# Kernel optimization log

Hardware: AMD Instinct MI355X
Metric: run time of the kernel (lower is better)

The kernel has to match this reference:

```python
import jax, jax.numpy as jnp
import numpy as np

N_NODES = 50000
N_EDGES = 800000
DIM = 128
NUM_GRAPHS = 512


def setup_inputs() -> dict:
    key = jax.random.key(0)
    ks = jax.random.split(key, 12)
    s = 1.0 / np.sqrt(DIM)
    inp = {
        'x': jax.random.normal(ks[0], (N_NODES, DIM), dtype=jnp.float32),
        'edge_index': jax.random.randint(ks[1], (2, N_EDGES), 0, N_NODES, dtype=jnp.int32),
        'batch': jnp.sort(jax.random.randint(ks[2], (N_NODES,), 0, NUM_GRAPHS, dtype=jnp.int32)),
        'W1a': jax.random.uniform(ks[3], (DIM, DIM), jnp.float32, -s, s),
        'b1a': jax.random.uniform(ks[4], (DIM,), jnp.float32, -s, s),
        'W1b': jax.random.uniform(ks[5], (DIM, DIM), jnp.float32, -s, s),
        'b1b': jax.random.uniform(ks[6], (DIM,), jnp.float32, -s, s),
        'W2a': jax.random.uniform(ks[7], (DIM, DIM), jnp.float32, -s, s),
        'b2a': jax.random.uniform(ks[8], (DIM,), jnp.float32, -s, s),
        'W2b': jax.random.uniform(ks[9], (DIM, DIM), jnp.float32, -s, s),
        'b2b': jax.random.uniform(ks[10], (DIM,), jnp.float32, -s, s),
    }
    return inp


def _gin_conv(x, edge_index, Wa, ba, Wb, bb):
    # GINConv with eps=0: h_i = MLP(x_i + sum_{j->i} x_j)
    src, dst = edge_index[0], edge_index[1]
    agg = jax.ops.segment_sum(x[src], dst, num_segments=x.shape[0])  # [N, F]
    h = x + agg
    h = jax.nn.relu(h @ Wa + ba)
    return h @ Wb + bb


def reference(x, edge_index, batch, W1a, b1a, W1b, b1b, W2a, b2a, W2b, b2b):
    h = _gin_conv(x, edge_index, W1a, b1a, W1b, b1b)
    h = _gin_conv(h, edge_index, W2a, b2a, W2b, b2b)
    # global mean pool over graphs
    sums = jax.ops.segment_sum(h, batch, num_segments=NUM_GRAPHS)      # [G, F]
    counts = jax.ops.segment_sum(jnp.ones((h.shape[0],), h.dtype), batch, num_segments=NUM_GRAPHS)
    return sums / jnp.maximum(counts, 1.0)[:, None]
```

## Files before the change

### kernel.cpp

```cpp
#include <hip/hip_runtime.h>

#define DIM 128
#define NBUCK 784
#define EPB 8192
#define ELDS_CAP 2048

typedef unsigned short ushortT;
typedef unsigned int uintT;
typedef __attribute__((ext_vector_type(8))) __bf16 bf16x8;
typedef __attribute__((ext_vector_type(4))) float f32x4;

__device__ inline ushortT f2bf(float f) {
    union { float f; uintT u; } v; v.f = f;
    uintT u = v.u;
    uintT r = (u + 0x7FFFu + ((u >> 16) & 1u)) >> 16;
    return (ushortT)r;
}
__device__ inline float bfu_lo(uintT u) { union { uintT u; float f; } v; v.u = u << 16; return v.f; }
__device__ inline float bfu_hi(uintT u) { union { uintT u; float f; } v; v.u = u & 0xffff0000u; return v.f; }
__device__ inline float bfs(ushortT s) { union { uintT u; float f; } v; v.u = ((uintT)s) << 16; return v.f; }

__device__ inline int off_in_row(int k) {
    return (((k >> 5) * 4 + ((k & 15) >> 2)) << 4) + (((k >> 4) & 1) << 3) + ((k & 3) << 1);
}

__device__ inline int wave_iscan(int v) {
    int lane = threadIdx.x & 63;
    #pragma unroll
    for (int d = 1; d < 64; d <<= 1) {
        int t = __shfl_up(v, d, 64);
        if (lane >= d) v += t;
    }
    return v;
}

__global__ __launch_bounds__(256)
void scan_blk_kernel(int* __restrict__ a, int n, int* __restrict__ bsum) {
    __shared__ int ws[4];
    const int tid = threadIdx.x;
    const int i = blockIdx.x * 256 + tid;
    const int lane = tid & 63, wv = tid >> 6;
    int v = (i < n) ? a[i] : 0;
    int isc = wave_iscan(v);
    if (lane == 63) ws[wv] = isc;
    __syncthreads();
    if (tid == 0) { int run = 0; for (int w = 0; w < 4; ++w) { int t = ws[w]; ws[w] = run; run += t; } }
    __syncthreads();
    int e = ws[wv] + isc - v;
    if (i < n) a[i] = e;
    if (tid == 255) bsum[blockIdx.x] = e + v;
}

__global__ __launch_bounds__(256)
void scan_add2_kernel(int* __restrict__ a, int n, const int* __restrict__ bsum) {
    __shared__ int ws[4];
    __shared__ int s_carry;
    const int tid = threadIdx.x;
    int partial = 0;
    for (int i = tid; i < (int)blockIdx.x; i += 256) partial += bsum[i];
    #pragma unroll
    for (int d = 1; d < 64; d <<= 1) partial += __shfl_xor(partial, d, 64);
    if ((tid & 63) == 0) ws[tid >> 6] = partial;
    __syncthreads();
    if (tid == 0) s_carry = ws[0] + ws[1] + ws[2] + ws[3];
    __syncthreads();
    int i = blockIdx.x * 256 + tid;
    if (i < n) a[i] += s_carry;
}

__global__ __launch_bounds__(256)
void histA_kernel(const int* __restrict__ dstIdx, int* __restrict__ histg, int ne, int nblk) {
    __shared__ int h[NBUCK];
    const int j = blockIdx.x;
    for (int i = threadIdx.x; i < NBUCK; i += 256) h[i] = 0;
    __syncthreads();
    const int base = j * EPB;
    const int end = (base + EPB < ne) ? base + EPB : ne;
    for (int i = base + threadIdx.x; i < end; i += 256)
        atomicAdd(&h[dstIdx[i] >> 6], 1);
    __syncthreads();
    for (int b = threadIdx.x; b < NBUCK; b += 256)
        histg[b * nblk + j] = h[b];
}

__global__ __launch_bounds__(256)
void fillA_kernel(const int* __restrict__ srcIdx, const int* __restrict__ dstIdx,
                  const int* __restrict__ Sg, uintT* __restrict__ pairs, int ne, int nblk) {
    __shared__ int cur[NBUCK];
    const int j = blockIdx.x;
    for (int i = threadIdx.x; i < NBUCK; i += 256) cur[i] = Sg[i * nblk + j];
    __syncthreads();
    const int base = j * EPB;
    const int end = (base + EPB < ne) ? base + EPB : ne;
    for (int i = base + threadIdx.x; i < end; i += 256) {
        const int d = dstIdx[i];
        const int b = d >> 6;
        const int pos = atomicAdd(&cur[b], 1);
        pairs[pos] = ((uintT)srcIdx[i] << 6) | (uintT)(d & 63);
    }
}

__global__ __launch_bounds__(256)
void convert_prep_kernel(const float* __restrict__ x, ushortT* __restrict__ xb, int n,
                         const float* __restrict__ W0, const float* __restrict__ W1,
                         const float* __restrict__ W2, const float* __restrict__ W3,
                         ushortT* __restrict__ Wt) {
    if (blockIdx.x < 128) {
        int w = blockIdx.x >> 5;
        const float* W = (w == 0) ? W0 : (w == 1) ? W1 : (w == 2) ? W2 : W3;
        ushortT* dst = Wt + (size_t)w * DIM * DIM;
        int i = (blockIdx.x & 31) * 256 + threadIdx.x;
        int nidx = i >> 6, p = i & 63, k = 2 * p;
        float w0 = W[k * DIM + nidx];
        float w1 = W[(k + 1) * DIM + nidx];
        uintT u = ((uintT)f2bf(w1) << 16) | f2bf(w0);
        *(uintT*)((char*)dst + (size_t)nidx * 256 + (off_in_row(k) ^ ((nidx & 7) << 4))) = u;
        return;
    }
    int i = (blockIdx.x - 128) * 256 + threadIdx.x;
    int node = i >> 6, p = i & 63;
    if (node >= n) return;
    float2 v = *(const float2*)(x + (size_t)node * DIM + 2 * p);
    uintT u = ((uintT)f2bf(v.y) << 16) | f2bf(v.x);
    *(uintT*)((char*)xb + (size_t)node * 256 + (off_in_row(2 * p) ^ ((node & 7) << 4))) = u;
}

__global__ __launch_bounds__(128)
void graphoff_zero_kernel(const int* __restrict__ batch, int* __restrict__ goff,
                          float* __restrict__ out, int ng, int nn) {
    const int g = blockIdx.x;
    out[(size_t)g * DIM + threadIdx.x] = 0.0f;
    if (threadIdx.x == 0) {
        int lo = 0, hi = nn;
        while (lo < hi) { int mid = (lo + hi) >> 1; if (batch[mid] < g) lo = mid + 1; else hi = mid; }
        goff[g] = lo;
    }
}

template<int POOL>
__global__ __launch_bounds__(512, 4)
void fused_kernel(const ushortT* __restrict__ Xsrc, ushortT* __restrict__ Yg,
                  const uintT* __restrict__ pairs, const int* __restrict__ Sg, int nblk,
                  const ushortT* __restrict__ WtA, const float* __restrict__ ba,
                  const ushortT* __restrict__ WtB, const float* __restrict__ bb,
                  const int* __restrict__ batch, float* __restrict__ out, int n, int ne) {
    __shared__ __align__(16) ushortT XsU[64 * DIM];
    __shared__ int elds[ELDS_CAP];
    __shared__ int histc[64];
    __shared__ int lstart[65];
    __shared__ int bs[64];

    const int b = blockIdx.x;
    const int node0 = b * 64;
    const int tid = threadIdx.x;
    const int lane = tid & 63, wid = tid >> 6;

    const int base = Sg[b * nblk];
    const int endp = (b + 1 < NBUCK) ? Sg[(b + 1) * nblk] : ne;
    int cnt = endp - base;
    if (cnt > ELDS_CAP) cnt = ELDS_CAP;

    if (tid < 64) {
        histc[tid] = 0;
        if (POOL) { int node = node0 + tid; bs[tid] = (node < n) ? batch[node] : -1; }
    }
    __syncthreads();
    for (int i = tid; i < cnt; i += 512) atomicAdd(&histc[pairs[base + i] & 63], 1);
    __syncthreads();
    if (tid < 64) {
        int v = histc[tid];
        int isc = wave_iscan(v);
        lstart[tid] = isc - v;
        histc[tid] = isc - v;
        if (tid == 63) lstart[64] = isc;
    }
    __syncthreads();
    for (int i = tid; i < cnt; i += 512) {
        uintT p = pairs[base + i];
        int pos = atomicAdd(&histc[p & 63], 1);
        elds[pos] = (int)(p >> 6);
    }
    __syncthreads();

    const int l15 = lane & 15, g16 = lane >> 4;
    const char* Xc = (const char*)Xsrc;
    for (int t = 0; t < 8; ++t) {
        const int r = wid * 8 + t;
        const int node = node0 + r;
        float acc[8];
        #pragma unroll
        for (int j = 0; j < 8; ++j) acc[j] = 0.0f;
        if (node < n) {
            if (g16 == 0) {
                uint4 v = *(const uint4*)(Xc + (size_t)node * 256 + ((l15 ^ (node & 7)) << 4));
                acc[0] += bfu_lo(v.x); acc[1] += bfu_hi(v.x);
                acc[2] += bfu_lo(v.y); acc[3] += bfu_hi(v.y);
                acc[4] += bfu_lo(v.z); acc[5] += bfu_hi(v.z);
                acc[6] += bfu_lo(v.w); acc[7] += bfu_hi(v.w);
            }
            const int s0 = lstart[r], s1 = lstart[r + 1];
            int e = s0;
            for (; e + 8 <= s1; e += 8) {
                const int sa = elds[e + g16];
                const int sb = elds[e + 4 + g16];
                uint4 va = *(const uint4*)(Xc + (size_t)sa * 256 + ((l15 ^ (sa & 7)) << 4));
                uint4 vb = *(const uint4*)(Xc + (size_t)sb * 256 + ((l15 ^ (sb & 7)) << 4));
                acc[0] += bfu_lo(va.x) + bfu_lo(vb.x); acc[1] += bfu_hi(va.x) + bfu_hi(vb.x);
                acc[2] += bfu_lo(va.y) + bfu_lo(vb.y); acc[3] += bfu_hi(va.y) + bfu_hi(vb.y);
                acc[4] += bfu_lo(va.z) + bfu_lo(vb.z); acc[5] += bfu_hi(va.z) + bfu_hi(vb.z);
                acc[6] += bfu_lo(va.w) + bfu_lo(vb.w); acc[7] += bfu_hi(va.w) + bfu_hi(vb.w);
            }
            if (e + 4 <= s1) {
                const int s = elds[e + g16];
                uint4 v = *(const uint4*)(Xc + (size_t)s * 256 + ((l15 ^ (s & 7)) << 4));
                acc[0] += bfu_lo(v.x); acc[1] += bfu_hi(v.x);
                acc[2] += bfu_lo(v.y); acc[3] += bfu_hi(v.y);
                acc[4] += bfu_lo(v.z); acc[5] += bfu_hi(v.z);
                acc[6] += bfu_lo(v.w); acc[7] += bfu_hi(v.w);
                e += 4;
            }
            const int rem = s1 - e;
            if (g16 < rem) {
                const int s = elds[e + g16];
                uint4 v = *(const uint4*)(Xc + (size_t)s * 256 + ((l15 ^ (s & 7)) << 4));
                acc[0] += bfu_lo(v.x); acc[1] += bfu_hi(v.x);
                acc[2] += bfu_lo(v.y); acc[3] += bfu_hi(v.y);
                acc[4] += bfu_lo(v.z); acc[5] += bfu_hi(v.z);
                acc[6] += bfu_lo(v.w); acc[7] += bfu_hi(v.w);
            }
        }
        #pragma unroll
        for (int j = 0; j < 8; ++j) {
            acc[j] += __shfl_xor(acc[j], 16);
            acc[j] += __shfl_xor(acc[j], 32);
        }
        if (lane < 16) {
            uint4 o;
            o.x = ((uintT)f2bf(acc[1]) << 16) | f2bf(acc[0]);
            o.y = ((uintT)f2bf(acc[3]) << 16) | f2bf(acc[2]);
            o.z = ((uintT)f2bf(acc[5]) << 16) | f2bf(acc[4]);
            o.w = ((uintT)f2bf(acc[7]) << 16) | f2bf(acc[6]);
            *(uint4*)((char*)XsU + r * 256 + ((l15 ^ (r & 7)) << 4)) = o;
        }
    }
    __syncthreads();

    const char* Xl = (const char*)XsU;
    const char* Wa = (const char*)WtA;
    const char* Wb = (const char*)WtB;
    const int g = lane >> 4;
    const int RB = (wid >> 2) * 32, CB = (wid & 3) * 32;

    f32x4 acc2[2][2];
    #pragma unroll
    for (int nt = 0; nt < 2; ++nt) {
        float bv = ba[CB + nt * 16 + l15];
        #pragma unroll
        for (int mt = 0; mt < 2; ++mt) acc2[mt][nt] = (f32x4){bv, bv, bv, bv};
    }
    #pragma unroll
    for (int ks = 0; ks < 4; ++ks) {
        const int cb = (ks * 4 + g) << 4;
        bf16x8 a0, a1, bf[2];
        { int r0 = RB + l15, r1 = RB + 16 + l15;
          a0 = *(const bf16x8*)(Xl + r0 * 256 + (cb ^ ((r0 & 7) << 4)));
          a1 = *(const bf16x8*)(Xl + r1 * 256 + (cb ^ ((r1 & 7) << 4))); }
        #pragma unroll
        for (int nt = 0; nt < 2; ++nt) {
            int rn = CB + nt * 16 + l15;
            bf[nt] = *(const bf16x8*)(Wa + rn * 256 + (cb ^ ((rn & 7) << 4)));
        }
        #pragma unroll
        for (int nt = 0; nt < 2; ++nt) {
            acc2[0][nt] = __builtin_amdgcn_mfma_f32_16x16x32_bf16(a0, bf[nt], acc2[0][nt], 0, 0, 0);
            acc2[1][nt] = __builtin_amdgcn_mfma_f32_16x16x32_bf16(a1, bf[nt], acc2[1][nt], 0, 0, 0);
        }
    }
    #pragma unroll
    for (int mt = 0; mt < 2; ++mt)
        #pragma unroll
        for (int nt = 0; nt < 2; ++nt)
            #pragma unroll
            for (int c = 0; c < 4; ++c) acc2[mt][nt][c] = fmaxf(acc2[mt][nt][c], 0.0f);

    __syncthreads();

    #pragma unroll
    for (int nt = 0; nt < 2; ++nt) {
        const int k = CB + nt * 16 + l15;
        const int offk = off_in_row(k);
        #pragma unroll
        for (int mt = 0; mt < 2; ++mt)
            #pragma unroll
            for (int r = 0; r < 4; ++r) {
                int row = RB + mt * 16 + 4 * g + r;
                *(ushortT*)((char*)XsU + row * 256 + (offk ^ ((row & 7) << 4))) = f2bf(acc2[mt][nt][r]);
            }
    }
    __syncthreads();

    #pragma unroll
    for (int nt = 0; nt < 2; ++nt) {
        float bv = bb[CB + nt * 16 + l15];
        #pragma unroll
        for (int mt = 0; mt < 2; ++mt) acc2[mt][nt] = (f32x4){bv, bv, bv, bv};
    }
    #pragma unroll
    for (int ks = 0; ks < 4; ++ks) {
        const int cb = (ks * 4 + g) << 4;
        bf16x8 a0, a1, bf[2];
        { int r0 = RB + l15, r1 = RB + 16 + l15;
          a0 = *(const bf16x8*)(Xl + r0 * 256 + (cb ^ ((r0 & 7) << 4)));
          a1 = *(const bf16x8*)(Xl + r1 * 256 + (cb ^ ((r1 & 7) << 4))); }
        #pragma unroll
        for (int nt = 0; nt < 2; ++nt) {
            int rn = CB + nt * 16 + l15;
            bf[nt] = *(const bf16x8*)(Wb + rn * 256 + (cb ^ ((rn & 7) << 4)));
        }
        #pragma unroll
        for (int nt = 0; nt < 2; ++nt) {
            acc2[0][nt] = __builtin_amdgcn_mfma_f32_16x16x32_bf16(a0, bf[nt], acc2[0][nt], 0, 0, 0);
            acc2[1][nt] = __builtin_amdgcn_mfma_f32_16x16x32_bf16(a1, bf[nt], acc2[1][nt], 0, 0, 0);
        }
    }

    if (POOL) {
        __syncthreads();
        #pragma unroll
        for (int nt = 0; nt < 2; ++nt) {
            const int k = CB + nt * 16 + l15;
            const int offk = off_in_row(k);
            #pragma unroll
            for (int mt = 0; mt < 2; ++mt)
                #pragma unroll
                for (int r = 0; r < 4; ++r) {
                    int row = RB + mt * 16 + 4 * g + r;
                    *(ushortT*)((char*)XsU + row * 256 + (offk ^ ((row & 7) << 4))) = f2bf(acc2[mt][nt][r]);
                }
        }
        __syncthreads();
        const int col = tid & 127, rh = tid >> 7;
        const int offc = off_in_row(col);
        const int r0 = rh * 16, r1 = r0 + 16;
        float run = 0.0f;
        int gcur = bs[r0];
        for (int r = r0; r < r1; ++r) {
            int gb = bs[r];
            if (gb != gcur) {
                if (gcur >= 0) atomicAdd(&out[(size_t)gcur * DIM + col], run);
                run = 0.0f; gcur = gb;
            }
            run += bfs(*(const ushortT*)((const char*)XsU + r * 256 + (offc ^ ((r & 7) << 4))));
        }
        if (gcur >= 0) atomicAdd(&out[(size_t)gcur * DIM + col], run);
    } else {
        #pragma unroll
        for (int nt = 0; nt < 2; ++nt) {
            const int k = CB + nt * 16 + l15;
            const int offk = off_in_row(k);
            #pragma unroll
            for (int mt = 0; mt < 2; ++mt)
                #pragma unroll
                for (int r = 0; r < 4; ++r) {
                    int row = RB + mt * 16 + 4 * g + r;
                    int node = node0 + row;
                    if (node < n)
                        *(ushortT*)((char*)Yg + (size_t)node * 256 + (offk ^ ((row & 7) << 4))) = f2bf(acc2[mt][nt][r]);
                }
        }
    }
}

__global__ __launch_bounds__(256)
void divide_kernel(float* __restrict__ out, const int* __restrict__ goff, int ng, int nn) {
    int i = blockIdx.x * 256 + threadIdx.x;
    if (i >= ng * DIM) return;
    int gidx = i >> 7;
    int cnt = ((gidx + 1 < ng) ? goff[gidx + 1] : nn) - goff[gidx];
    out[i] /= fmaxf((float)cnt, 1.0f);
}

extern "C" void kernel_launch(void* const* d_in, const int* in_sizes, int n_in,
                              void* d_out, int out_size, void* d_ws, size_t ws_size,
                              hipStream_t stream) {
    const float* x     = (const float*)d_in[0];
    const int*   ei    = (const int*)d_in[1];
    const int*   batch = (const int*)d_in[2];
    const float* W1a = (const float*)d_in[3];
    const float* b1a = (const float*)d_in[4];
    const float* W1b = (const float*)d_in[5];
    const float* b1b = (const float*)d_in[6];
    const float* W2a = (const float*)d_in[7];
    const float* b2a = (const float*)d_in[8];
    const float* W2b = (const float*)d_in[9];
    const float* b2b = (const float*)d_in[10];
    float* out = (float*)d_out;

    const int NN = in_sizes[0] / DIM;
    const int NE = in_sizes[1] / 2;
    const int NG = out_size / DIM;
    const int NN2 = (NN + 63) & ~63;
    const int nblk = (NE + EPB - 1) / EPB;
    const int nS = NBUCK * nblk;
    const int nScanBlk = (nS + 255) / 256;

    ushortT* xb    = (ushortT*)d_ws;
    ushortT* bufB  = xb   + (size_t)NN2 * DIM;
    ushortT* wt    = bufB + (size_t)NN2 * DIM;
    uintT*   pairs = (uintT*)(wt + 4 * DIM * DIM);
    int*     Sg    = (int*)(pairs + (size_t)NE);
    int*     bsum  = Sg + nS;
    int*     goff  = bsum + nScanBlk;

    const int* srcIdx = ei;
    const int* dstIdx = ei + NE;

    histA_kernel<<<nblk, 256, 0, stream>>>(dstIdx, Sg, NE, nblk);
    scan_blk_kernel<<<nScanBlk, 256, 0, stream>>>(Sg, nS, bsum);
    scan_add2_kernel<<<nScanBlk, 256, 0, stream>>>(Sg, nS, bsum);
    fillA_kernel<<<nblk, 256, 0, stream>>>(srcIdx, dstIdx, Sg, pairs, NE, nblk);

    convert_prep_kernel<<<128 + (NN * 64) / 256, 256, 0, stream>>>(x, xb, NN, W1a, W1b, W2a, W2b, wt);
    graphoff_zero_kernel<<<NG, 128, 0, stream>>>(batch, goff, out, NG, NN);

    fused_kernel<0><<<NBUCK, 512, 0, stream>>>(xb, bufB, pairs, Sg, nblk,
                                               wt, b1a, wt + DIM * DIM, b1b,
                                               batch, out, NN, NE);
    fused_kernel<1><<<NBUCK, 512, 0, stream>>>(bufB, (ushortT*)nullptr, pairs, Sg, nblk,
                                               wt + 2 * DIM * DIM, b2a, wt + 3 * DIM * DIM, b2b,
                                               batch, out, NN, NE);

    divide_kernel<<<(out_size + 255) / 256, 256, 0, stream>>>(out, goff, NG, NN);
}
```

Before: 140.8 us.

## Switch node features to fp16 with packed half accumulation and precomputed gather offsets

Node features and weights are now stored as fp16 instead of bf16. The neighbor gather accumulates with packed f16x2 adds rather than unpacking each value to fp32, and the MFMA calls use the f16 variant. Edge pairs now carry a precomputed swizzled byte offset, so the gather loop drops per-edge address arithmetic, and that loop is unrolled to 16 edges with two accumulator sets. The cost is lower accumulation precision: summing about 16 neighbors in half precision risks rounding error or overflow for large activations.

```diff
diff --git a/kernel.cpp b/kernel.cpp
--- a/kernel.cpp
+++ b/kernel.cpp
@@ -7,21 +7,23 @@
 
 typedef unsigned short ushortT;
 typedef unsigned int uintT;
-typedef __attribute__((ext_vector_type(8))) __bf16 bf16x8;
+typedef _Float16 f16;
+typedef __attribute__((ext_vector_type(2))) _Float16 f16x2;
+typedef __attribute__((ext_vector_type(8))) _Float16 f16x8;
 typedef __attribute__((ext_vector_type(4))) float f32x4;
 
-__device__ inline ushortT f2bf(float f) {
-    union { float f; uintT u; } v; v.f = f;
-    uintT u = v.u;
-    uintT r = (u + 0x7FFFu + ((u >> 16) & 1u)) >> 16;
-    return (ushortT)r;
-}
-__device__ inline float bfu_lo(uintT u) { union { uintT u; float f; } v; v.u = u << 16; return v.f; }
-__device__ inline float bfu_hi(uintT u) { union { uintT u; float f; } v; v.u = u & 0xffff0000u; return v.f; }
-__device__ inline float bfs(ushortT s) { union { uintT u; float f; } v; v.u = ((uintT)s) << 16; return v.f; }
+__device__ inline ushortT f2h(float f) { return __builtin_bit_cast(ushortT, (f16)f); }
+__device__ inline float h2f(ushortT s) { return (float)__builtin_bit_cast(f16, s); }
 
 __device__ inline int off_in_row(int k) {
     return (((k >> 5) * 4 + ((k & 15) >> 2)) << 4) + (((k >> 4) & 1) << 3) + ((k & 3) << 1);
+}
+
+__device__ inline void add4(f16x2* a, uint4 v) {
+    a[0] += __builtin_bit_cast(f16x2, v.x);
+    a[1] += __builtin_bit_cast(f16x2, v.y);
+    a[2] += __builtin_bit_cast(f16x2, v.z);
+    a[3] += __builtin_bit_cast(f16x2, v.w);
 }
 
 __device__ inline int wave_iscan(int v) {
@@ -94,9 +96,11 @@
     const int end = (base + EPB < ne) ? base + EPB : ne;
     for (int i = base + threadIdx.x; i < end; i += 256) {
         const int d = dstIdx[i];
+        const int s = srcIdx[i];
         const int b = d >> 6;
+        const uintT E4 = ((uintT)s << 4) ^ (uintT)(s & 7);
         const int pos = atomicAdd(&cur[b], 1);
-        pairs[pos] = ((uintT)srcIdx[i] << 6) | (uintT)(d & 63);
+        pairs[pos] = (E4 << 6) | (uintT)(d & 63);
     }
 }
 
@@ -113,7 +117,7 @@
         int nidx = i >> 6, p = i & 63, k = 2 * p;
         float w0 = W[k * DIM + nidx];
         float w1 = W[(k + 1) * DIM + nidx];
-        uintT u = ((uintT)f2bf(w1) << 16) | f2bf(w0);
+        uintT u = ((uintT)f2h(w1) << 16) | f2h(w0);
         *(uintT*)((char*)dst + (size_t)nidx * 256 + (off_in_row(k) ^ ((nidx & 7) << 4))) = u;
         return;
     }
@@ -121,7 +125,7 @@
     int node = i >> 6, p = i & 63;
     if (node >= n) return;
     float2 v = *(const float2*)(x + (size_t)node * DIM + 2 * p);
-    uintT u = ((uintT)f2bf(v.y) << 16) | f2bf(v.x);
+    uintT u = ((uintT)f2h(v.y) << 16) | f2h(v.x);
     *(uintT*)((char*)xb + (size_t)node * 256 + (off_in_row(2 * p) ^ ((node & 7) << 4))) = u;
 }
 
@@ -178,69 +182,61 @@
     for (int i = tid; i < cnt; i += 512) {
         uintT p = pairs[base + i];
         int pos = atomicAdd(&histc[p & 63], 1);
-        elds[pos] = (int)(p >> 6);
+        elds[pos] = (int)((p >> 6) << 4);
     }
     __syncthreads();
 
     const int l15 = lane & 15, g16 = lane >> 4;
+    const int lofs = l15 << 4;
     const char* Xc = (const char*)Xsrc;
     for (int t = 0; t < 8; ++t) {
         const int r = wid * 8 + t;
         const int node = node0 + r;
-        float acc[8];
-        #pragma unroll
-        for (int j = 0; j < 8; ++j) acc[j] = 0.0f;
+        f16x2 a0[4], a1[4];
+        #pragma unroll
+        for (int j = 0; j < 4; ++j) { a0[j] = (f16x2)0; a1[j] = (f16x2)0; }
         if (node < n) {
             if (g16 == 0) {
-                uint4 v = *(const uint4*)(Xc + (size_t)node * 256 + ((l15 ^ (node & 7)) << 4));
-                acc[0] += bfu_lo(v.x); acc[1] += bfu_hi(v.x);
-                acc[2] += bfu_lo(v.y); acc[3] += bfu_hi(v.y);
-                acc[4] += bfu_lo(v.z); acc[5] += bfu_hi(v.z);
-                acc[6] += bfu_lo(v.w); acc[7] += bfu_hi(v.w);
+                const int Es = (node << 8) ^ ((node & 7) << 4);
+                add4(a0, *(const uint4*)(Xc + (Es ^ lofs)));
             }
             const int s0 = lstart[r], s1 = lstart[r + 1];
             int e = s0;
-            for (; e + 8 <= s1; e += 8) {
-                const int sa = elds[e + g16];
-                const int sb = elds[e + 4 + g16];
-                uint4 va = *(const uint4*)(Xc + (size_t)sa * 256 + ((l15 ^ (sa & 7)) << 4));
-                uint4 vb = *(const uint4*)(Xc + (size_t)sb * 256 + ((l15 ^ (sb & 7)) << 4));
-                acc[0] += bfu_lo(va.x) + bfu_lo(vb.x); acc[1] += bfu_hi(va.x) + bfu_hi(vb.x);
-                acc[2] += bfu_lo(va.y) + bfu_lo(vb.y); acc[3] += bfu_hi(va.y) + bfu_hi(vb.y);
-                acc[4] += bfu_lo(va.z) + bfu_lo(vb.z); acc[5] += bfu_hi(va.z) + bfu_hi(vb.z);
-                acc[6] += bfu_lo(va.w) + bfu_lo(vb.w); acc[7] += bfu_hi(va.w) + bfu_hi(vb.w);
-            }
-            if (e + 4 <= s1) {
-                const int s = elds[e + g16];
-                uint4 v = *(const uint4*)(Xc + (size_t)s * 256 + ((l15 ^ (s & 7)) << 4));
-                acc[0] += bfu_lo(v.x); acc[1] += bfu_hi(v.x);
-                acc[2] += bfu_lo(v.y); acc[3] += bfu_hi(v.y);
-                acc[4] += bfu_lo(v.z); acc[5] += bfu_hi(v.z);
-                acc[6] += bfu_lo(v.w); acc[7] += bfu_hi(v.w);
-                e += 4;
+            for (; e + 16 <= s1; e += 16) {
+                const int Ea = elds[e + g16];
+                const int Eb = elds[e + 4 + g16];
+                const int Ec = elds[e + 8 + g16];
+                const int Ed = elds[e + 12 + g16];
+                uint4 va = *(const uint4*)(Xc + (Ea ^ lofs));
+                uint4 vb = *(const uint4*)(Xc + (Eb ^ lofs));
+                uint4 vc = *(const uint4*)(Xc + (Ec ^ lofs));
+                uint4 vd = *(const uint4*)(Xc + (Ed ^ lofs));
+                add4(a0, va); add4(a1, vb); add4(a0, vc); add4(a1, vd);
+            }
+            for (; e + 4 <= s1; e += 4) {
+                const int E = elds[e + g16];
+                add4(a0, *(const uint4*)(Xc + (E ^ lofs)));
             }
             const int rem = s1 - e;
             if (g16 < rem) {
-                const int s = elds[e + g16];
-                uint4 v = *(const uint4*)(Xc + (size_t)s * 256 + ((l15 ^ (s & 7)) << 4));
-                acc[0] += bfu_lo(v.x); acc[1] += bfu_hi(v.x);
-                acc[2] += bfu_lo(v.y); acc[3] += bfu_hi(v.y);
-                acc[4] += bfu_lo(v.z); acc[5] += bfu_hi(v.z);
-                acc[6] += bfu_lo(v.w); acc[7] += bfu_hi(v.w);
-            }
-        }
-        #pragma unroll
-        for (int j = 0; j < 8; ++j) {
-            acc[j] += __shfl_xor(acc[j], 16);
-            acc[j] += __shfl_xor(acc[j], 32);
+                const int E = elds[e + g16];
+                add4(a1, *(const uint4*)(Xc + (E ^ lofs)));
+            }
+        }
+        #pragma unroll
+        for (int j = 0; j < 4; ++j) a0[j] += a1[j];
+        #pragma unroll
+        for (int j = 0; j < 4; ++j) {
+            a0[j] += __builtin_bit_cast(f16x2, __shfl_xor(__builtin_bit_cast(int, a0[j]), 16));
+            a0[j] += __builtin_bit_cast(f16x2, __shfl_xor(__builtin_bit_cast(int, a0[j]), 32));
         }
         if (lane < 16) {
             uint4 o;
-            o.x = ((uintT)f2bf(acc[1]) << 16) | f2bf(acc[0]);
-            o.y = ((uintT)f2bf(acc[3]) << 16) | f2bf(acc[2]);
-            o.z = ((uintT)f2bf(acc[5]) << 16) | f2bf(acc[4]);
-            o.w = ((uintT)f2bf(acc[7]) << 16) | f2bf(acc[6]);
-            *(uint4*)((char*)XsU + r * 256 + ((l15 ^ (r & 7)) << 4)) = o;
+            o.x = __builtin_bit_cast(uintT, a0[0]);
+            o.y = __builtin_bit_cast(uintT, a0[1]);
+            o.z = __builtin_bit_cast(uintT, a0[2]);
+            o.w = __builtin_bit_cast(uintT, a0[3]);
+            *(uint4*)((char*)XsU + ((r << 8) ^ (lofs ^ ((r & 7) << 4)))) = o;
         }
     }
     __syncthreads();
@@ -261,19 +257,19 @@
     #pragma unroll
     for (int ks = 0; ks < 4; ++ks) {
         const int cb = (ks * 4 + g) << 4;
-        bf16x8 a0, a1, bf[2];
+        f16x8 a0, a1, bf[2];
         { int r0 = RB + l15, r1 = RB + 16 + l15;
-          a0 = *(const bf16x8*)(Xl + r0 * 256 + (cb ^ ((r0 & 7) << 4)));
-          a1 = *(const bf16x8*)(Xl + r1 * 256 + (cb ^ ((r1 & 7) << 4))); }
+          a0 = *(const f16x8*)(Xl + r0 * 256 + (cb ^ ((r0 & 7) << 4)));
+          a1 = *(const f16x8*)(Xl + r1 * 256 + (cb ^ ((r1 & 7) << 4))); }
         #pragma unroll
         for (int nt = 0; nt < 2; ++nt) {
             int rn = CB + nt * 16 + l15;
-            bf[nt] = *(const bf16x8*)(Wa + rn * 256 + (cb ^ ((rn & 7) << 4)));
-        }
-        #pragma unroll
-        for (int nt = 0; nt < 2; ++nt) {
-            acc2[0][nt] = __builtin_amdgcn_mfma_f32_16x16x32_bf16(a0, bf[nt], acc2[0][nt], 0, 0, 0);
-            acc2[1][nt] = __builtin_amdgcn_mfma_f32_16x16x32_bf16(a1, bf[nt], acc2[1][nt], 0, 0, 0);
+            bf[nt] = *(const f16x8*)(Wa + rn * 256 + (cb ^ ((rn & 7) << 4)));
+        }
+        #pragma unroll
+        for (int nt = 0; nt < 2; ++nt) {
+            acc2[0][nt] = __builtin_amdgcn_mfma_f32_16x16x32_f16(a0, bf[nt], acc2[0][nt], 0, 0, 0);
+            acc2[1][nt] = __builtin_amdgcn_mfma_f32_16x16x32_f16(a1, bf[nt], acc2[1][nt], 0, 0, 0);
         }
     }
     #pragma unroll
@@ -294,7 +290,7 @@
             #pragma unroll
             for (int r = 0; r < 4; ++r) {
                 int row = RB + mt * 16 + 4 * g + r;
-                *(ushortT*)((char*)XsU + row * 256 + (offk ^ ((row & 7) << 4))) = f2bf(acc2[mt][nt][r]);
+                *(ushortT*)((char*)XsU + row * 256 + (offk ^ ((row & 7) << 4))) = f2h(acc2[mt][nt][r]);
             }
     }
     __syncthreads();
@@ -308,19 +304,19 @@
     #pragma unroll
     for (int ks = 0; ks < 4; ++ks) {
         const int cb = (ks * 4 + g) << 4;
-        bf16x8 a0, a1, bf[2];
+        f16x8 a0, a1, bf[2];
         { int r0 = RB + l15, r1 = RB + 16 + l15;
-          a0 = *(const bf16x8*)(Xl + r0 * 256 + (cb ^ ((r0 & 7) << 4)));
-          a1 = *(const bf16x8*)(Xl + r1 * 256 + (cb ^ ((r1 & 7) << 4))); }
+          a0 = *(const f16x8*)(Xl + r0 * 256 + (cb ^ ((r0 & 7) << 4)));
+          a1 = *(const f16x8*)(Xl + r1 * 256 + (cb ^ ((r1 & 7) << 4))); }
         #pragma unroll
         for (int nt = 0; nt < 2; ++nt) {
             int rn = CB + nt * 16 + l15;
-            bf[nt] = *(const bf16x8*)(Wb + rn * 256 + (cb ^ ((rn & 7) << 4)));
-        }
-        #pragma unroll
-        for (int nt = 0; nt < 2; ++nt) {
-            acc2[0][nt] = __builtin_amdgcn_mfma_f32_16x16x32_bf16(a0, bf[nt], acc2[0][nt], 0, 0, 0);
-            acc2[1][nt] = __builtin_amdgcn_mfma_f32_16x16x32_bf16(a1, bf[nt], acc2[1][nt], 0, 0, 0);
+            bf[nt] = *(const f16x8*)(Wb + rn * 256 + (cb ^ ((rn & 7) << 4)));
+        }
+        #pragma unroll
+        for (int nt = 0; nt < 2; ++nt) {
+            acc2[0][nt] = __builtin_amdgcn_mfma_f32_16x16x32_f16(a0, bf[nt], acc2[0][nt], 0, 0, 0);
+            acc2[1][nt] = __builtin_amdgcn_mfma_f32_16x16x32_f16(a1, bf[nt], acc2[1][nt], 0, 0, 0);
         }
     }
 
@@ -335,7 +331,7 @@
                 #pragma unroll
                 for (int r = 0; r < 4; ++r) {
                     int row = RB + mt * 16 + 4 * g + r;
-                    *(ushortT*)((char*)XsU + row * 256 + (offk ^ ((row & 7) << 4))) = f2bf(acc2[mt][nt][r]);
+                    *(ushortT*)((char*)XsU + row * 256 + (offk ^ ((row & 7) << 4))) = f2h(acc2[mt][nt][r]);
                 }
         }
         __syncthreads();
@@ -350,7 +346,7 @@
                 if (gcur >= 0) atomicAdd(&out[(size_t)gcur * DIM + col], run);
                 run = 0.0f; gcur = gb;
             }
-            run += bfs(*(const ushortT*)((const char*)XsU + r * 256 + (offc ^ ((r & 7) << 4))));
+            run += h2f(*(const ushortT*)((const char*)XsU + r * 256 + (offc ^ ((r & 7) << 4))));
         }
         if (gcur >= 0) atomicAdd(&out[(size_t)gcur * DIM + col], run);
     } else {
@@ -365,7 +361,7 @@
                     int row = RB + mt * 16 + 4 * g + r;
                     int node = node0 + row;
                     if (node < n)
-                        *(ushortT*)((char*)Yg + (size_t)node * 256 + (offk ^ ((row & 7) << 4))) = f2bf(acc2[mt][nt][r]);
+                        *(ushortT*)((char*)Yg + (size_t)node * 256 + (offk ^ ((row & 7) << 4))) = f2h(acc2[mt][nt][r]);
                 }
         }
     }
```

New measurement: 130.5 us. 1.08x faster.
